# Kernel optimization log

Measured on AMD Instinct MI355X. Metric: run time of the kernel, lower is better.

Reference implementation:

```python
import jax, jax.numpy as jnp
import numpy as np

N0, N1, N2 = 200000, 50000, 10000
D_IN, D_PROMPT, D_HID, D_OUT = 128, 64, 256, 2
E0, E1 = 800000, 160000


def _glorot(key, shape):
    fan_in, fan_out = shape[0], shape[1]
    lim = np.sqrt(6.0 / (fan_in + fan_out))
    return jax.random.uniform(key, shape, jnp.float32, -lim, lim)


def setup_inputs() -> dict:
    key = jax.random.key(0)
    ks = jax.random.split(key, 20)
    inp = {
        "features": jax.random.normal(ks[0], (N0, D_IN), jnp.float32),
        "membership_mask": jax.random.randint(ks[1], (N0,), 0, 2) > 0,
        "src0": jax.random.randint(ks[2], (E0,), 0, N0),
        "dst0": jax.random.randint(ks[3], (E0,), 0, N1),
        "src1": jax.random.randint(ks[4], (E1,), 0, N1),
        "dst1": jax.random.randint(ks[5], (E1,), 0, N2),
        "output_nodes_indices": jax.random.randint(ks[6], (N2,), 0, N2),
        # prompt MLPs
        "w_pin": _glorot(ks[7], (D_IN, D_PROMPT)),
        "b_pin": jnp.zeros((D_PROMPT,), jnp.float32),
        "w_pout": _glorot(ks[8], (D_IN, D_PROMPT)),
        "b_pout": jnp.zeros((D_PROMPT,), jnp.float32),
        # SAGEConv layer 0: (D_IN+D_PROMPT) -> D_HID
        "w_self0": _glorot(ks[9], (D_IN + D_PROMPT, D_HID)),
        "w_neigh0": _glorot(ks[10], (D_IN + D_PROMPT, D_HID)),
        "b0": jnp.zeros((D_HID,), jnp.float32),
        # SAGEConv layer 1: D_HID -> D_HID
        "w_self1": _glorot(ks[11], (D_HID, D_HID)),
        "w_neigh1": _glorot(ks[12], (D_HID, D_HID)),
        "b1": jnp.zeros((D_HID,), jnp.float32),
        # classifier
        "w_cls": _glorot(ks[13], (D_HID, D_OUT)),
        "b_cls": jnp.zeros((D_OUT,), jnp.float32),
    }
    return inp


def _sage_mean(h, src, dst, n_dst, w_self, w_neigh, b):
    # mean-aggregate src features into dst buckets (zero-degree -> 0, DGL semantics)
    agg = jax.ops.segment_sum(h[src], dst, num_segments=n_dst)
    deg = jax.ops.segment_sum(jnp.ones((src.shape[0],), h.dtype), dst, num_segments=n_dst)
    agg = agg / jnp.maximum(deg, 1.0)[:, None]
    return h[:n_dst] @ w_self + agg @ w_neigh + b


def reference(features, membership_mask, src0, dst0, src1, dst1, output_nodes_indices,
              w_pin, b_pin, w_pout, b_pout,
              w_self0, w_neigh0, b0, w_self1, w_neigh1, b1, w_cls, b_cls):
    p_in = jax.nn.relu(features @ w_pin + b_pin)
    p_out = jax.nn.relu(features @ w_pout + b_pout)
    sel = jnp.where(membership_mask[:, None], p_in, p_out)
    h = jnp.concatenate([features, sel], axis=1)          # [N0, D_IN+D_PROMPT]
    h = jax.nn.relu(_sage_mean(h, src0, dst0, N1, w_self0, w_neigh0, b0))  # [N1, D_HID]
    h = _sage_mean(h, src1, dst1, N2, w_self1, w_neigh1, b1)               # [N2, D_HID]
    logits = h @ w_cls + b_cls                             # [N2, D_OUT]
    return logits
```

## Files before the change

### kernel.cpp

```cpp
#include <hip/hip_runtime.h>


#define N0v 200000
#define N1v 50000
#define N2v 10000
#define E0v 800000
#define E1v 160000
#define TB0 49
#define TB1 10
#define TBL (TB0 + TB1)

using u16 = unsigned short;
typedef __attribute__((ext_vector_type(8))) short short8;
typedef __attribute__((ext_vector_type(4))) float f32x4;

__device__ __forceinline__ float b2f(u16 u) {
    union { unsigned int i; float f; } v; v.i = ((unsigned int)u) << 16; return v.f;
}
__device__ __forceinline__ u16 f2b(float f) {
    union { float f; unsigned int i; } v; v.f = f;
    return (u16)((v.i + 0x7fffu + ((v.i >> 16) & 1u)) >> 16);
}
__device__ __forceinline__ void split2(float f, u16& h, u16& l) {
    h = f2b(f);
    l = f2b(f - b2f(h));
}

__global__ void k_prep(const unsigned* mask, int* flag,
                       const float* w_pin, const float* w_pout, u16* WTph, u16* WTpl,
                       const float* ws0, const float* wn0, u16* WT0h, u16* WT0l,
                       const float* ws1, const float* wn1, u16* WT1h, u16* WT1l,
                       const float* bc, float* outp,
                       const int* __restrict__ dst0, const int* __restrict__ dst1,
                       int* cnt0, int* cnt1, int* rk0, int* rk1) {
    const int R0 = 50000;
    const int R1 = R0 + 128 * 128;
    const int R2 = R1 + 256 * 384;
    const int R3 = R2 + 256 * 512;
    const int R4 = R3 + 2 * N2v;
    const int R5 = R4 + E0v;
    const int R6 = R5 + E1v;
    for (int i = blockIdx.x * blockDim.x + threadIdx.x; i < R6;
         i += gridDim.x * blockDim.x) {
        if (i < R0) {
            if (mask[i] > 1u) atomicOr(flag, 1);
        } else if (i < R1) {
            int j = i - R0, n = j >> 7, k = j & 127;
            float f = (n < 64) ? w_pin[k * 64 + n] : w_pout[k * 64 + (n - 64)];
            split2(f, WTph[j], WTpl[j]);
        } else if (i < R2) {
            int j = i - R1, n = j / 384, k = j % 384;
            float f = (k < 192) ? ws0[k * 256 + n] : wn0[(k - 192) * 256 + n];
            split2(f, WT0h[j], WT0l[j]);
        } else if (i < R3) {
            int j = i - R2, n = j >> 9, k = j & 511;
            float f = (k < 256) ? ws1[k * 256 + n] : wn1[(k - 256) * 256 + n];
            split2(f, WT1h[j], WT1l[j]);
        } else if (i < R4) {
            int j = i - R3;
            outp[j] = bc[j & 1];
        } else if (i < R5) {
            int e = i - R4;
            rk0[e] = atomicAdd(&cnt0[dst0[e]], 1);
        } else {
            int e = i - R5;
            rk1[e] = atomicAdd(&cnt1[dst1[e]], 1);
        }
    }
}

__global__ __launch_bounds__(256) void k_scan_a(const int* __restrict__ cnt0,
                                                int* __restrict__ off0,
                                                const int* __restrict__ cnt1,
                                                int* __restrict__ off1,
                                                int* __restrict__ tsum) {
    __shared__ int sd[256];
    const int t = threadIdx.x;
    const int blk = blockIdx.x;
    const int g1 = (blk >= TB0);
    const int b = g1 ? blk - TB0 : blk;
    const int n = g1 ? N2v : N1v;
    const int* cnt = g1 ? cnt1 : cnt0;
    int* off = g1 ? off1 : off0;
    const int i0 = b * 1024 + t * 4;
    int c[4] = {0, 0, 0, 0};
    if (i0 + 3 < n) {
        *(int4*)c = *(const int4*)&cnt[i0];
    } else {
        for (int j = 0; j < 4; j++) if (i0 + j < n) c[j] = cnt[i0 + j];
    }
    int s = c[0] + c[1] + c[2] + c[3];
    sd[t] = s;
    __syncthreads();
#pragma unroll
    for (int d = 1; d < 256; d <<= 1) {
        int v = (t >= d) ? sd[t - d] : 0;
        __syncthreads();
        sd[t] += v;
        __syncthreads();
    }
    int run = sd[t] - s;
    int o4[4];
#pragma unroll
    for (int j = 0; j < 4; j++) { o4[j] = run; run += c[j]; }
    if (i0 + 3 < n) *(int4*)&off[i0] = *(const int4*)o4;
    else for (int j = 0; j < 4; j++) if (i0 + j < n) off[i0 + j] = o4[j];
    if (t == 255) tsum[blk] = sd[255];
}

__global__ __launch_bounds__(256) void k_scan_c(int* __restrict__ off0,
                                                int* __restrict__ off1,
                                                const int* __restrict__ tsum) {
    __shared__ int lbase;
    const int t = threadIdx.x;
    const int blk = blockIdx.x;
    const int g1 = (blk >= TB0);
    const int b = g1 ? blk - TB0 : blk;
    const int n = g1 ? N2v : N1v;
    int* off = g1 ? off1 : off0;
    if (t < 64) {
        int v = (t < TBL) ? tsum[t] : 0;
        int incl = v;
#pragma unroll
        for (int d = 1; d < 64; d <<= 1) {
            int u = __shfl_up(incl, d);
            if (t >= d) incl += u;
        }
        int total0 = __shfl(incl, TB0 - 1);
        if (t == blk) lbase = (incl - v) - (g1 ? total0 : 0);
    }
    __syncthreads();
    const int base = lbase;
    const int i0 = b * 1024 + t * 4;
    if (i0 + 3 < n) {
        int4 v = *(int4*)&off[i0];
        v.x += base; v.y += base; v.z += base; v.w += base;
        *(int4*)&off[i0] = v;
    } else {
        for (int j = 0; j < 4; j++) if (i0 + j < n) off[i0 + j] += base;
    }
    if (blk == 0 && t == 0) { off0[N1v] = E0v; off1[N2v] = E1v; }
}

__global__ __launch_bounds__(256) void k_scatter2(
    const int* __restrict__ src0, const int* __restrict__ dst0,
    const int* __restrict__ off0, const int* __restrict__ rk0, int* __restrict__ ei0,
    const int* __restrict__ src1, const int* __restrict__ dst1,
    const int* __restrict__ off1, const int* __restrict__ rk1, int* __restrict__ ei1) {
    const int part = blockIdx.x & 7;
    const int chunk = blockIdx.x >> 3;
    const int nch = gridDim.x >> 3;
    {
        const int per = (E0v + nch - 1) / nch;
        const int i1 = min((chunk + 1) * per, E0v);
        for (int i = chunk * per + (int)threadIdx.x; i < i1; i += 256) {
            int d = dst0[i];
            if (d / 6250 == part) ei0[off0[d] + rk0[i]] = src0[i];
        }
    }
    {
        const int per = (E1v + nch - 1) / nch;
        const int i1 = min((chunk + 1) * per, E1v);
        for (int i = chunk * per + (int)threadIdx.x; i < i1; i += 256) {
            int d = dst1[i];
            if (d / 1250 == part) ei1[off1[d] + rk1[i]] = src1[i];
        }
    }
}

__global__ __launch_bounds__(256, 4) void k_gemm_p(
    const float* __restrict__ A, const u16* __restrict__ Bh, const u16* __restrict__ Bl,
    const float* __restrict__ b_pin, const float* __restrict__ b_pout,
    const void* maskp, const int* __restrict__ flag, u16* __restrict__ G) {
    __shared__ __align__(16) u16 LA[8704];
    const int t = threadIdx.x;
    const int bm = blockIdx.x;
    const int lane = t & 63, w = t >> 6;
    const int m = lane & 15, q = lane >> 4;
    const int r0 = bm * 64;
    const int colbase = w * 32;

    const int fl = *flag;
    bool mk0, mk1;
    {
        const int ra = r0 + (t >> 3), rb = ra + 32;
        if (fl) {
            mk0 = ((const unsigned char*)maskp)[ra] != 0;
            mk1 = ((const unsigned char*)maskp)[rb] != 0;
        } else {
            mk0 = ((const int*)maskp)[ra] != 0;
            mk1 = ((const int*)maskp)[rb] != 0;
        }
    }

    const size_t ba = (size_t)(colbase + m) * 128 + q * 8;
    const size_t bb = (size_t)(colbase + 16 + m) * 128 + q * 8;
    short8 nb0h = *(const short8*)&Bh[ba];
    short8 nb0l = *(const short8*)&Bl[ba];
    short8 nb1h = *(const short8*)&Bh[bb];
    short8 nb1l = *(const short8*)&Bl[bb];

    {
        const int r15 = t >> 4, ch = t & 15;
        const int k0 = ch >> 2, q2 = ch & 3;
#pragma unroll
        for (int p = 0; p < 4; p++) {
            const int row = r0 + r15 + 16 * p;
            const float* ap = &A[(size_t)row * 128 + ch * 8];
            float4 v0 = *(const float4*)ap, v1 = *(const float4*)(ap + 4);
            u16 h8[8];
            h8[0] = f2b(v0.x); h8[1] = f2b(v0.y); h8[2] = f2b(v0.z); h8[3] = f2b(v0.w);
            h8[4] = f2b(v1.x); h8[5] = f2b(v1.y); h8[6] = f2b(v1.z); h8[7] = f2b(v1.w);
            *(uint4*)&G[(size_t)row * 192 + ch * 8] = *(const uint4*)h8;
            *(uint4*)&LA[((p * 4 + k0) * 66 + 16 * q2 + r15) * 8] = *(const uint4*)h8;
        }
    }
    __syncthreads();

    f32x4 acc[4][2] = {};
#pragma unroll
    for (int k0 = 0; k0 < 4; k0++) {
        short8 b0h = nb0h, b0l = nb0l, b1h = nb1h, b1l = nb1l;
        if (k0 < 3) {
            nb0h = *(const short8*)&Bh[ba + (k0 + 1) * 32];
            nb0l = *(const short8*)&Bl[ba + (k0 + 1) * 32];
            nb1h = *(const short8*)&Bh[bb + (k0 + 1) * 32];
            nb1l = *(const short8*)&Bl[bb + (k0 + 1) * 32];
        }
#pragma unroll
        for (int mi = 0; mi < 4; mi++) {
            short8 af = *(const short8*)&LA[((mi * 4 + k0) * 66 + lane) * 8];
            acc[mi][0] = __builtin_amdgcn_mfma_f32_16x16x32_bf16(af, b0h, acc[mi][0], 0, 0, 0);
            acc[mi][0] = __builtin_amdgcn_mfma_f32_16x16x32_bf16(af, b0l, acc[mi][0], 0, 0, 0);
            acc[mi][1] = __builtin_amdgcn_mfma_f32_16x16x32_bf16(af, b1h, acc[mi][1], 0, 0, 0);
            acc[mi][1] = __builtin_amdgcn_mfma_f32_16x16x32_bf16(af, b1l, acc[mi][1], 0, 0, 0);
        }
    }

    float bv[2];
#pragma unroll
    for (int nt = 0; nt < 2; nt++) {
        int col = colbase + nt * 16 + m;
        bv[nt] = (col < 64) ? b_pin[col] : b_pout[col - 64];
    }
    __syncthreads();
#pragma unroll
    for (int mi = 0; mi < 4; mi++)
#pragma unroll
        for (int nt = 0; nt < 2; nt++)
#pragma unroll
            for (int r = 0; r < 4; r++) {
                float v = acc[mi][nt][r] + bv[nt];
                v = v > 0.f ? v : 0.f;
                LA[(mi * 16 + q * 4 + r) * 136 + colbase + nt * 16 + m] = f2b(v);
            }
    __syncthreads();
    {
        const int c8 = t & 7;
        const int rt = t >> 3;
        *(uint4*)&G[(size_t)(r0 + rt) * 192 + 128 + c8 * 8] =
            *(const uint4*)&LA[rt * 136 + (mk0 ? 0 : 64) + c8 * 8];
        *(uint4*)&G[(size_t)(r0 + 32 + rt) * 192 + 128 + c8 * 8] =
            *(const uint4*)&LA[(32 + rt) * 136 + (mk1 ? 0 : 64) + c8 * 8];
    }
}

template <int MODE, int KT, int KE0, int MT>
__global__ __launch_bounds__(256, 3) void k_g(
    const u16* __restrict__ A0, int s0, const u16* __restrict__ A1, int s1,
    const u16* __restrict__ Bh, const u16* __restrict__ Bl,
    const float* __restrict__ bias,
    u16* __restrict__ CH, float* __restrict__ outp, const float* __restrict__ wc,
    int M) {
    constexpr int MI = MT / 16;
    __shared__ __align__(16) u16 LA[MI * KT * 66 * 8];
    const int t = threadIdx.x;
    const int bm = blockIdx.x >> 1, bn = blockIdx.x & 1;
    const int lane = t & 63, w = t >> 6;
    const int m = lane & 15, q = lane >> 4;
    const int r0 = bm * MT;
    const int colbase = bn * 128 + w * 32;
    const int K = KT * 32;

    {
        constexpr int TPR = 256 / MT;
        constexpr int SPT = KT / TPR;
        const int rr = t / TPR, sub = t & (TPR - 1);
        int arow = r0 + rr; if (arow >= M) arow = M - 1;
        const int mi = rr >> 4, r15 = rr & 15;
#pragma unroll
        for (int s = 0; s < SPT; s++) {
            const int kc = sub * SPT + s;
#pragma unroll
            for (int q2 = 0; q2 < 4; q2++) {
                const int c = kc * 32 + q2 * 8;
                uint4 v = (c < KE0 * 32)
                              ? *(const uint4*)&A0[(size_t)arow * s0 + c]
                              : *(const uint4*)&A1[(size_t)arow * s1 + (c - KE0 * 32)];
                *(uint4*)&LA[((mi * KT + kc) * 66 + 16 * q2 + r15) * 8] = v;
            }
        }
    }
    __syncthreads();

    const size_t ba = (size_t)(colbase + m) * K + q * 8;
    const size_t bb = (size_t)(colbase + 16 + m) * K + q * 8;

    f32x4 acc[MI][2] = {};
#pragma unroll 1
    for (int kb = 0; kb < KT; kb += 4) {
#pragma unroll
        for (int k0 = 0; k0 < 4; k0++) {
            const size_t ko = (size_t)(kb + k0) * 32;
            short8 b0h = *(const short8*)&Bh[ba + ko];
            short8 b0l = *(const short8*)&Bl[ba + ko];
            short8 b1h = *(const short8*)&Bh[bb + ko];
            short8 b1l = *(const short8*)&Bl[bb + ko];
#pragma unroll
            for (int mi = 0; mi < MI; mi++) {
                short8 af = *(const short8*)&LA[((mi * KT + kb + k0) * 66 + lane) * 8];
                acc[mi][0] = __builtin_amdgcn_mfma_f32_16x16x32_bf16(af, b0h, acc[mi][0], 0, 0, 0);
                acc[mi][0] = __builtin_amdgcn_mfma_f32_16x16x32_bf16(af, b0l, acc[mi][0], 0, 0, 0);
                acc[mi][1] = __builtin_amdgcn_mfma_f32_16x16x32_bf16(af, b1h, acc[mi][1], 0, 0, 0);
                acc[mi][1] = __builtin_amdgcn_mfma_f32_16x16x32_bf16(af, b1l, acc[mi][1], 0, 0, 0);
            }
        }
    }

    if (MODE == 1) {
        float bv[2];
#pragma unroll
        for (int nt = 0; nt < 2; nt++) bv[nt] = bias[colbase + nt * 16 + m];
        __syncthreads();
#pragma unroll
        for (int mi = 0; mi < MI; mi++)
#pragma unroll
            for (int nt = 0; nt < 2; nt++)
#pragma unroll
                for (int r = 0; r < 4; r++) {
                    float v = acc[mi][nt][r] + bv[nt];
                    v = v > 0.f ? v : 0.f;
                    LA[(mi * 16 + q * 4 + r) * 136 + w * 32 + nt * 16 + m] = f2b(v);
                }
        __syncthreads();
        const int c16 = t & 15;
#pragma unroll
        for (int pass = 0; pass < MT / 16; pass++) {
            const int rt = pass * 16 + (t >> 4);
            const int row = r0 + rt;
            if (row < M) {
                *(uint4*)&CH[(size_t)row * 256 + bn * 128 + c16 * 8] =
                    *(const uint4*)&LA[rt * 136 + c16 * 8];
            }
        }
    } else {
        const int ca = colbase + m, cb = colbase + 16 + m;
        const float bva = bias[ca], bvb = bias[cb];
        const float w0a = wc[ca * 2], w1a = wc[ca * 2 + 1];
        const float w0b = wc[cb * 2], w1b = wc[cb * 2 + 1];
#pragma unroll
        for (int mi = 0; mi < MI; mi++) {
#pragma unroll
            for (int r = 0; r < 4; r++) {
                int row = r0 + mi * 16 + q * 4 + r;
                float va = acc[mi][0][r] + bva;
                float vb = acc[mi][1][r] + bvb;
                float p0 = va * w0a + vb * w0b;
                float p1 = va * w1a + vb * w1b;
#pragma unroll
                for (int s = 1; s < 16; s <<= 1) {
                    p0 += __shfl_xor(p0, s);
                    p1 += __shfl_xor(p1, s);
                }
                if (m == 0 && row < M) {
                    atomicAdd(&outp[row * 2], p0);
                    atomicAdd(&outp[row * 2 + 1], p1);
                }
            }
        }
    }
}

__global__ void k_agg0(const u16* __restrict__ G, const int* __restrict__ off,
                       const int* __restrict__ eidx, u16* __restrict__ aggH) {
    int wid = (blockIdx.x * blockDim.x + threadIdx.x) >> 6;
    int lane = threadIdx.x & 63;
    if (wid >= N1v) return;
    int b = off[wid], e = off[wid + 1];
    float f0 = 0.f, f1 = 0.f, p0 = 0.f;
    for (int base = b; base < e; base += 64) {
        int li = base + lane;
        int idx = eidx[li < e ? li : (e - 1)];
        int nch = e - base; if (nch > 64) nch = 64;
        int j = 0;
        for (; j + 4 <= nch; j += 4) {
            int sa = __shfl(idx, j), sb = __shfl(idx, j + 1);
            int sc = __shfl(idx, j + 2), sd = __shfl(idx, j + 3);
            const u16* ra = &G[(size_t)sa * 192];
            const u16* rb = &G[(size_t)sb * 192];
            const u16* rc = &G[(size_t)sc * 192];
            const u16* rd = &G[(size_t)sd * 192];
            unsigned fa = *(const unsigned*)&ra[2 * lane];
            unsigned fb = *(const unsigned*)&rb[2 * lane];
            unsigned fc = *(const unsigned*)&rc[2 * lane];
            unsigned fd = *(const unsigned*)&rd[2 * lane];
            u16 pa = ra[128 + lane], pb = rb[128 + lane];
            u16 pc = rc[128 + lane], pd = rd[128 + lane];
            f0 += b2f((u16)fa) + b2f((u16)fb) + b2f((u16)fc) + b2f((u16)fd);
            f1 += b2f((u16)(fa >> 16)) + b2f((u16)(fb >> 16)) +
                  b2f((u16)(fc >> 16)) + b2f((u16)(fd >> 16));
            p0 += b2f(pa) + b2f(pb) + b2f(pc) + b2f(pd);
        }
        for (; j < nch; j++) {
            int s = __shfl(idx, j);
            const u16* row = &G[(size_t)s * 192];
            unsigned fv = *(const unsigned*)&row[2 * lane];
            f0 += b2f((u16)fv);
            f1 += b2f((u16)(fv >> 16));
            p0 += b2f(row[128 + lane]);
        }
    }
    int deg = e - b;
    float inv = 1.0f / (float)(deg > 1 ? deg : 1);
    size_t rb2 = (size_t)wid * 192;
    *(unsigned*)&aggH[rb2 + 2 * lane] =
        (unsigned)f2b(f0 * inv) | ((unsigned)f2b(f1 * inv) << 16);
    aggH[rb2 + 128 + lane] = f2b(p0 * inv);
}

__global__ void k_agg1(const u16* __restrict__ h1H, const int* __restrict__ off,
                       const int* __restrict__ eidx, u16* __restrict__ aggH) {
    int wid = (blockIdx.x * blockDim.x + threadIdx.x) >> 6;
    int lane = threadIdx.x & 63;
    if (wid >= N2v) return;
    int b = off[wid], e = off[wid + 1];
    float a0 = 0.f, a1 = 0.f, a2 = 0.f, a3 = 0.f;
    for (int base = b; base < e; base += 64) {
        int li = base + lane;
        int idx = eidx[li < e ? li : (e - 1)];
        int nch = e - base; if (nch > 64) nch = 64;
        int j = 0;
        for (; j + 4 <= nch; j += 4) {
            int sa = __shfl(idx, j), sb = __shfl(idx, j + 1);
            int sc = __shfl(idx, j + 2), sd = __shfl(idx, j + 3);
            const u16* ra = &h1H[(size_t)sa * 256];
            const u16* rb = &h1H[(size_t)sb * 256];
            const u16* rc = &h1H[(size_t)sc * 256];
            const u16* rd = &h1H[(size_t)sd * 256];
            unsigned va0 = *(const unsigned*)&ra[2 * lane];
            unsigned vb0 = *(const unsigned*)&rb[2 * lane];
            unsigned vc0 = *(const unsigned*)&rc[2 * lane];
            unsigned vd0 = *(const unsigned*)&rd[2 * lane];
            unsigned va1 = *(const unsigned*)&ra[128 + 2 * lane];
            unsigned vb1 = *(const unsigned*)&rb[128 + 2 * lane];
            unsigned vc1 = *(const unsigned*)&rc[128 + 2 * lane];
            unsigned vd1 = *(const unsigned*)&rd[128 + 2 * lane];
            a0 += b2f((u16)va0) + b2f((u16)vb0) + b2f((u16)vc0) + b2f((u16)vd0);
            a1 += b2f((u16)(va0 >> 16)) + b2f((u16)(vb0 >> 16)) +
                  b2f((u16)(vc0 >> 16)) + b2f((u16)(vd0 >> 16));
            a2 += b2f((u16)va1) + b2f((u16)vb1) + b2f((u16)vc1) + b2f((u16)vd1);
            a3 += b2f((u16)(va1 >> 16)) + b2f((u16)(vb1 >> 16)) +
                  b2f((u16)(vc1 >> 16)) + b2f((u16)(vd1 >> 16));
        }
        for (; j < nch; j++) {
            int s = __shfl(idx, j);
            const u16* row = &h1H[(size_t)s * 256];
            unsigned v0 = *(const unsigned*)&row[2 * lane];
            unsigned v1 = *(const unsigned*)&row[128 + 2 * lane];
            a0 += b2f((u16)v0); a1 += b2f((u16)(v0 >> 16));
            a2 += b2f((u16)v1); a3 += b2f((u16)(v1 >> 16));
        }
    }
    int deg = e - b;
    float inv = 1.0f / (float)(deg > 1 ? deg : 1);
    size_t rb2 = (size_t)wid * 256;
    *(unsigned*)&aggH[rb2 + 2 * lane] =
        (unsigned)f2b(a0 * inv) | ((unsigned)f2b(a1 * inv) << 16);
    *(unsigned*)&aggH[rb2 + 128 + 2 * lane] =
        (unsigned)f2b(a2 * inv) | ((unsigned)f2b(a3 * inv) << 16);
}

extern "C" void kernel_launch(void* const* d_in, const int* in_sizes, int n_in,
                              void* d_out, int out_size, void* d_ws, size_t ws_size,
                              hipStream_t stream) {
    const float* features = (const float*)d_in[0];
    const void* maskp     = d_in[1];
    const int* src0       = (const int*)d_in[2];
    const int* dst0       = (const int*)d_in[3];
    const int* src1       = (const int*)d_in[4];
    const int* dst1       = (const int*)d_in[5];
    const float* w_pin    = (const float*)d_in[7];
    const float* b_pin    = (const float*)d_in[8];
    const float* w_pout   = (const float*)d_in[9];
    const float* b_pout   = (const float*)d_in[10];
    const float* w_self0  = (const float*)d_in[11];
    const float* w_neigh0 = (const float*)d_in[12];
    const float* b0       = (const float*)d_in[13];
    const float* w_self1  = (const float*)d_in[14];
    const float* w_neigh1 = (const float*)d_in[15];
    const float* b1       = (const float*)d_in[16];
    const float* w_cls    = (const float*)d_in[17];
    const float* b_cls    = (const float*)d_in[18];
    float* out = (float*)d_out;
    (void)in_sizes; (void)n_in; (void)out_size; (void)ws_size;

    char* ws = (char*)d_ws;
    size_t o = 0;
    auto alloc = [&](size_t bytes) { size_t r = o; o += (bytes + 255) & ~(size_t)255; return r; };
    size_t o_flag = alloc(4);
    size_t o_cnt0 = alloc(N1v * 4);
    size_t o_cnt1 = alloc(N2v * 4);
    size_t zero_end = o;
    size_t o_G    = alloc((size_t)N0v * 192 * 2);
    size_t o_aggH = alloc((size_t)N1v * 192 * 2);
    size_t o_h1H  = alloc((size_t)N1v * 256 * 2);
    size_t o_ag1H = alloc((size_t)N2v * 256 * 2);
    size_t o_wtph = alloc(128 * 128 * 2), o_wtpl = alloc(128 * 128 * 2);
    size_t o_wt0h = alloc(256 * 384 * 2), o_wt0l = alloc(256 * 384 * 2);
    size_t o_wt1h = alloc(256 * 512 * 2), o_wt1l = alloc(256 * 512 * 2);
    size_t o_off0 = alloc((N1v + 1) * 4);
    size_t o_off1 = alloc((N2v + 1) * 4);
    size_t o_ei0  = alloc((size_t)E0v * 4);
    size_t o_ei1  = alloc((size_t)E1v * 4);
    size_t o_rk0  = alloc((size_t)E0v * 4);
    size_t o_rk1  = alloc((size_t)E1v * 4);
    size_t o_tsum = alloc(TBL * 4);

    int* flag = (int*)(ws + o_flag);
    int* cnt0 = (int*)(ws + o_cnt0);
    int* cnt1 = (int*)(ws + o_cnt1);
    u16* G     = (u16*)(ws + o_G);
    u16* aggH  = (u16*)(ws + o_aggH);
    u16* h1H   = (u16*)(ws + o_h1H);
    u16* ag1H  = (u16*)(ws + o_ag1H);
    u16* WTph = (u16*)(ws + o_wtph);
    u16* WTpl = (u16*)(ws + o_wtpl);
    u16* WT0h = (u16*)(ws + o_wt0h);
    u16* WT0l = (u16*)(ws + o_wt0l);
    u16* WT1h = (u16*)(ws + o_wt1h);
    u16* WT1l = (u16*)(ws + o_wt1l);
    int* off0 = (int*)(ws + o_off0);
    int* off1 = (int*)(ws + o_off1);
    int* ei0  = (int*)(ws + o_ei0);
    int* ei1  = (int*)(ws + o_ei1);
    int* rk0  = (int*)(ws + o_rk0);
    int* rk1  = (int*)(ws + o_rk1);
    int* tsum = (int*)(ws + o_tsum);

    hipMemsetAsync(ws + o_flag, 0, zero_end - o_flag, stream);

    k_prep<<<1024, 256, 0, stream>>>((const unsigned*)maskp, flag,
                                     w_pin, w_pout, WTph, WTpl,
                                     w_self0, w_neigh0, WT0h, WT0l,
                                     w_self1, w_neigh1, WT1h, WT1l,
                                     b_cls, out, dst0, dst1, cnt0, cnt1, rk0, rk1);

    k_scan_a<<<TBL, 256, 0, stream>>>(cnt0, off0, cnt1, off1, tsum);
    k_scan_c<<<TBL, 256, 0, stream>>>(off0, off1, tsum);

    k_scatter2<<<2048, 256, 0, stream>>>(src0, dst0, off0, rk0, ei0,
                                         src1, dst1, off1, rk1, ei1);

    k_gemm_p<<<N0v / 64, 256, 0, stream>>>(features, WTph, WTpl,
                                           b_pin, b_pout, maskp, flag, G);

    k_agg0<<<(N1v + 3) / 4, 256, 0, stream>>>(G, off0, ei0, aggH);

    k_g<1, 12, 6, 64><<<((N1v + 63) / 64) * 2, 256, 0, stream>>>(
        G, 192, aggH, 192, WT0h, WT0l, b0, h1H, nullptr, nullptr, N1v);

    k_agg1<<<(N2v + 3) / 4, 256, 0, stream>>>(h1H, off1, ei1, ag1H);

    k_g<3, 16, 8, 32><<<((N2v + 31) / 32) * 2, 256, 0, stream>>>(
        h1H, 256, ag1H, 256, WT1h, WT1l, b1, nullptr, out, w_cls, N2v);
}
```

Before: 422.0 us.

## Stop materializing bf16 features copy; read fp32 features directly in agg and GEMM

```diff
diff --git a/kernel.cpp b/kernel.cpp
--- a/kernel.cpp
+++ b/kernel.cpp
@@ -193,40 +193,38 @@
         }
     }
 
-    const size_t ba = (size_t)(colbase + m) * 128 + q * 8;
-    const size_t bb = (size_t)(colbase + 16 + m) * 128 + q * 8;
-    short8 nb0h = *(const short8*)&Bh[ba];
-    short8 nb0l = *(const short8*)&Bl[ba];
-    short8 nb1h = *(const short8*)&Bh[bb];
-    short8 nb1l = *(const short8*)&Bl[bb];
-
     {
         const int r15 = t >> 4, ch = t & 15;
         const int k0 = ch >> 2, q2 = ch & 3;
+        const float* ap = &A[(size_t)(r0 + r15) * 128 + ch * 8];
+        float4 va[8];
 #pragma unroll
         for (int p = 0; p < 4; p++) {
-            const int row = r0 + r15 + 16 * p;
-            const float* ap = &A[(size_t)row * 128 + ch * 8];
-            float4 v0 = *(const float4*)ap, v1 = *(const float4*)(ap + 4);
+            va[2 * p]     = *(const float4*)(ap + (size_t)p * 16 * 128);
+            va[2 * p + 1] = *(const float4*)(ap + (size_t)p * 16 * 128 + 4);
+        }
+#pragma unroll
+        for (int p = 0; p < 4; p++) {
             u16 h8[8];
-            h8[0] = f2b(v0.x); h8[1] = f2b(v0.y); h8[2] = f2b(v0.z); h8[3] = f2b(v0.w);
-            h8[4] = f2b(v1.x); h8[5] = f2b(v1.y); h8[6] = f2b(v1.z); h8[7] = f2b(v1.w);
-            *(uint4*)&G[(size_t)row * 192 + ch * 8] = *(const uint4*)h8;
+            h8[0] = f2b(va[2 * p].x); h8[1] = f2b(va[2 * p].y);
+            h8[2] = f2b(va[2 * p].z); h8[3] = f2b(va[2 * p].w);
+            h8[4] = f2b(va[2 * p + 1].x); h8[5] = f2b(va[2 * p + 1].y);
+            h8[6] = f2b(va[2 * p + 1].z); h8[7] = f2b(va[2 * p + 1].w);
             *(uint4*)&LA[((p * 4 + k0) * 66 + 16 * q2 + r15) * 8] = *(const uint4*)h8;
         }
     }
     __syncthreads();
 
+    const size_t ba = (size_t)(colbase + m) * 128 + q * 8;
+    const size_t bb = (size_t)(colbase + 16 + m) * 128 + q * 8;
+
     f32x4 acc[4][2] = {};
 #pragma unroll
     for (int k0 = 0; k0 < 4; k0++) {
-        short8 b0h = nb0h, b0l = nb0l, b1h = nb1h, b1l = nb1l;
-        if (k0 < 3) {
-            nb0h = *(const short8*)&Bh[ba + (k0 + 1) * 32];
-            nb0l = *(const short8*)&Bl[ba + (k0 + 1) * 32];
-            nb1h = *(const short8*)&Bh[bb + (k0 + 1) * 32];
-            nb1l = *(const short8*)&Bl[bb + (k0 + 1) * 32];
-        }
+        short8 b0h = *(const short8*)&Bh[ba + k0 * 32];
+        short8 b0l = *(const short8*)&Bl[ba + k0 * 32];
+        short8 b1h = *(const short8*)&Bh[bb + k0 * 32];
+        short8 b1l = *(const short8*)&Bl[bb + k0 * 32];
 #pragma unroll
         for (int mi = 0; mi < 4; mi++) {
             short8 af = *(const short8*)&LA[((mi * 4 + k0) * 66 + lane) * 8];
@@ -258,15 +256,16 @@
     {
         const int c8 = t & 7;
         const int rt = t >> 3;
-        *(uint4*)&G[(size_t)(r0 + rt) * 192 + 128 + c8 * 8] =
+        *(uint4*)&G[(size_t)(r0 + rt) * 64 + c8 * 8] =
             *(const uint4*)&LA[rt * 136 + (mk0 ? 0 : 64) + c8 * 8];
-        *(uint4*)&G[(size_t)(r0 + 32 + rt) * 192 + 128 + c8 * 8] =
+        *(uint4*)&G[(size_t)(r0 + 32 + rt) * 64 + c8 * 8] =
             *(const uint4*)&LA[(32 + rt) * 136 + (mk1 ? 0 : 64) + c8 * 8];
     }
 }
 
-template <int MODE, int KT, int KE0, int MT>
+template <int MODE, int KT, int SEGF, int SEGA0, int MT>
 __global__ __launch_bounds__(256, 3) void k_g(
+    const float* __restrict__ Af,
     const u16* __restrict__ A0, int s0, const u16* __restrict__ A1, int s1,
     const u16* __restrict__ Bh, const u16* __restrict__ Bl,
     const float* __restrict__ bias,
@@ -294,9 +293,27 @@
 #pragma unroll
             for (int q2 = 0; q2 < 4; q2++) {
                 const int c = kc * 32 + q2 * 8;
-                uint4 v = (c < KE0 * 32)
-                              ? *(const uint4*)&A0[(size_t)arow * s0 + c]
-                              : *(const uint4*)&A1[(size_t)arow * s1 + (c - KE0 * 32)];
+                uint4 v;
+                if constexpr (SEGF > 0) {
+                    if (c < SEGF) {
+                        const float* ap = &Af[(size_t)arow * SEGF + c];
+                        float4 v0 = *(const float4*)ap, v1 = *(const float4*)(ap + 4);
+                        u16 h8[8];
+                        h8[0] = f2b(v0.x); h8[1] = f2b(v0.y);
+                        h8[2] = f2b(v0.z); h8[3] = f2b(v0.w);
+                        h8[4] = f2b(v1.x); h8[5] = f2b(v1.y);
+                        h8[6] = f2b(v1.z); h8[7] = f2b(v1.w);
+                        v = *(const uint4*)h8;
+                    } else if (c < SEGA0) {
+                        v = *(const uint4*)&A0[(size_t)arow * s0 + (c - SEGF)];
+                    } else {
+                        v = *(const uint4*)&A1[(size_t)arow * s1 + (c - SEGA0)];
+                    }
+                } else {
+                    v = (c < SEGA0)
+                            ? *(const uint4*)&A0[(size_t)arow * s0 + c]
+                            : *(const uint4*)&A1[(size_t)arow * s1 + (c - SEGA0)];
+                }
                 *(uint4*)&LA[((mi * KT + kc) * 66 + 16 * q2 + r15) * 8] = v;
             }
         }
@@ -381,7 +398,8 @@
     }
 }
 
-__global__ void k_agg0(const u16* __restrict__ G, const int* __restrict__ off,
+__global__ void k_agg0(const float* __restrict__ F, const u16* __restrict__ Gp,
+                       const int* __restrict__ off,
                        const int* __restrict__ eidx, u16* __restrict__ aggH) {
     int wid = (blockIdx.x * blockDim.x + threadIdx.x) >> 6;
     int lane = threadIdx.x & 63;
@@ -396,28 +414,22 @@
         for (; j + 4 <= nch; j += 4) {
             int sa = __shfl(idx, j), sb = __shfl(idx, j + 1);
             int sc = __shfl(idx, j + 2), sd = __shfl(idx, j + 3);
-            const u16* ra = &G[(size_t)sa * 192];
-            const u16* rb = &G[(size_t)sb * 192];
-            const u16* rc = &G[(size_t)sc * 192];
-            const u16* rd = &G[(size_t)sd * 192];
-            unsigned fa = *(const unsigned*)&ra[2 * lane];
-            unsigned fb = *(const unsigned*)&rb[2 * lane];
-            unsigned fc = *(const unsigned*)&rc[2 * lane];
-            unsigned fd = *(const unsigned*)&rd[2 * lane];
-            u16 pa = ra[128 + lane], pb = rb[128 + lane];
-            u16 pc = rc[128 + lane], pd = rd[128 + lane];
-            f0 += b2f((u16)fa) + b2f((u16)fb) + b2f((u16)fc) + b2f((u16)fd);
-            f1 += b2f((u16)(fa >> 16)) + b2f((u16)(fb >> 16)) +
-                  b2f((u16)(fc >> 16)) + b2f((u16)(fd >> 16));
+            float2 fa = *(const float2*)&F[(size_t)sa * 128 + 2 * lane];
+            float2 fb = *(const float2*)&F[(size_t)sb * 128 + 2 * lane];
+            float2 fc = *(const float2*)&F[(size_t)sc * 128 + 2 * lane];
+            float2 fd = *(const float2*)&F[(size_t)sd * 128 + 2 * lane];
+            u16 pa = Gp[(size_t)sa * 64 + lane], pb = Gp[(size_t)sb * 64 + lane];
+            u16 pc = Gp[(size_t)sc * 64 + lane], pd = Gp[(size_t)sd * 64 + lane];
+            f0 += fa.x + fb.x + fc.x + fd.x;
+            f1 += fa.y + fb.y + fc.y + fd.y;
             p0 += b2f(pa) + b2f(pb) + b2f(pc) + b2f(pd);
         }
         for (; j < nch; j++) {
             int s = __shfl(idx, j);
-            const u16* row = &G[(size_t)s * 192];
-            unsigned fv = *(const unsigned*)&row[2 * lane];
-            f0 += b2f((u16)fv);
-            f1 += b2f((u16)(fv >> 16));
-            p0 += b2f(row[128 + lane]);
+            float2 fv = *(const float2*)&F[(size_t)s * 128 + 2 * lane];
+            f0 += fv.x;
+            f1 += fv.y;
+            p0 += b2f(Gp[(size_t)s * 64 + lane]);
         }
     }
     int deg = e - b;
@@ -511,7 +523,7 @@
     size_t o_cnt0 = alloc(N1v * 4);
     size_t o_cnt1 = alloc(N2v * 4);
     size_t zero_end = o;
-    size_t o_G    = alloc((size_t)N0v * 192 * 2);
+    size_t o_G    = alloc((size_t)N0v * 64 * 2);
     size_t o_aggH = alloc((size_t)N1v * 192 * 2);
     size_t o_h1H  = alloc((size_t)N1v * 256 * 2);
     size_t o_ag1H = alloc((size_t)N2v * 256 * 2);
@@ -564,13 +576,13 @@
     k_gemm_p<<<N0v / 64, 256, 0, stream>>>(features, WTph, WTpl,
                                            b_pin, b_pout, maskp, flag, G);
 
-    k_agg0<<<(N1v + 3) / 4, 256, 0, stream>>>(G, off0, ei0, aggH);
-
-    k_g<1, 12, 6, 64><<<((N1v + 63) / 64) * 2, 256, 0, stream>>>(
-        G, 192, aggH, 192, WT0h, WT0l, b0, h1H, nullptr, nullptr, N1v);
+    k_agg0<<<(N1v + 3) / 4, 256, 0, stream>>>(features, G, off0, ei0, aggH);
+
+    k_g<1, 12, 128, 192, 64><<<((N1v + 63) / 64) * 2, 256, 0, stream>>>(
+        features, G, 64, aggH, 192, WT0h, WT0l, b0, h1H, nullptr, nullptr, N1v);
 
     k_agg1<<<(N2v + 3) / 4, 256, 0, stream>>>(h1H, off1, ei1, ag1H);
 
-    k_g<3, 16, 8, 32><<<((N2v + 31) / 32) * 2, 256, 0, stream>>>(
-        h1H, 256, ag1H, 256, WT1h, WT1l, b1, nullptr, out, w_cls, N2v);
-}
+    k_g<3, 16, 0, 256, 32><<<((N2v + 31) / 32) * 2, 256, 0, stream>>>(
+        nullptr, h1H, 256, ag1H, 256, WT1h, WT1l, b1, nullptr, out, w_cls, N2v);
+}
```

Result: slower. 462.2 us (+9.5%).
